# Kernel optimization log

Measured on AMD Instinct MI355X. Metric: run time of the kernel, lower is better.

Reference implementation:

```python
import jax, jax.numpy as jnp
import numpy as np


def setup_inputs() -> dict:
    key = jax.random.key(0)
    bs, width, length = 4, 1536, 2048  # width = 3 * num_heads * ch = 3*8*64
    qkv = jax.random.normal(key, (bs, width, length), dtype=jnp.float32)
    return {"qkv": qkv, "num_heads": 8}


def reference(qkv, num_heads):
    bs, width, length = qkv.shape
    assert width % (3 * num_heads) == 0
    ch = width // (3 * num_heads)
    q, k, v = jnp.split(qkv, 3, axis=1)  # each [bs, num_heads*ch, length]
    scale = 1.0 / np.sqrt(np.sqrt(ch))  # applied to both q and k (total 1/sqrt(ch))
    q = (q * scale).reshape(bs * num_heads, ch, length)
    k = (k * scale).reshape(bs * num_heads, ch, length)
    v = v.reshape(bs * num_heads, ch, length)
    # weight[b, t, s] = sum_c q[b,c,t] * k[b,c,s]
    weight = jnp.einsum('bct,bcs->bts', q, k)
    weight = jax.nn.softmax(weight.astype(jnp.float32), axis=-1).astype(weight.dtype)
    # a[b, c, t] = sum_s weight[b,t,s] * v[b,c,s]
    a = jnp.einsum('bts,bcs->bct', weight, v)
    return a.reshape(bs, num_heads * ch, length)
```

## Files before the change

kernel.cpp:

```cpp
#include <hip/hip_runtime.h>

typedef float f32x16 __attribute__((ext_vector_type(16)));
typedef short short8 __attribute__((ext_vector_type(8)));
typedef unsigned short u16;
typedef unsigned int u32;

#define SEQ_L 2048

#if __has_builtin(__builtin_amdgcn_exp2f)
#define EXP2(x) __builtin_amdgcn_exp2f(x)
#else
#define EXP2(x) exp2f(x)
#endif

__device__ __forceinline__ u32 pk2bf(float lo, float hi) {
#if __has_builtin(__builtin_amdgcn_cvt_pk_bf16_f32)
    typedef __bf16 bf16x2_t __attribute__((ext_vector_type(2)));
    union { bf16x2_t v; u32 i; } w;
    w.v = __builtin_amdgcn_cvt_pk_bf16_f32(lo, hi);
    return w.i;
#else
    union { float f; u32 i; } a, b; a.f = lo; b.f = hi;
    return ((a.i + 0x8000u) >> 16) | ((b.i + 0x8000u) & 0xFFFF0000u);
#endif
}

#define KT_U16 (64 * 64)
#define VT_STRIDE 72
#define VT_U16 (64 * VT_STRIDE)
#define GRP_U16 (KT_U16 + VT_U16)

__global__ __launch_bounds__(512, 4)
void attn_kernel(const float* __restrict__ qkv, float* __restrict__ out) {
    const int tid  = threadIdx.x;
    const int lane = tid & 63;
    const int wv   = tid >> 6;
    const int g    = wv >> 2;
    const int wvin = wv & 3;
    const int col  = lane & 31;
    const int half = lane >> 5;

    const int gid  = blockIdx.x;
    const int head = gid & 31;
    const int tb   = gid >> 5;
    const int t0   = tb * 128 + wvin * 32;
    const int bb   = head >> 3, hh = head & 7;

    const size_t qoff = ((size_t)bb * 1536 + (size_t)hh * 64) * SEQ_L;
    const float* qp = qkv + qoff;
    const float* kp = qp + (size_t)512  * SEQ_L;
    const float* vp = qp + (size_t)1024 * SEQ_L;
    float* op = out + ((size_t)bb * 512 + (size_t)hh * 64) * SEQ_L;

    __shared__ __align__(16) char smem[2 * GRP_U16 * 2];
    u16* ktg = (u16*)smem + g * GRP_U16;
    u16* vtg = ktg + KT_U16;

    const int gtid = tid & 255;
    const int sgrp = gtid & 15;
    const int rq   = gtid >> 4;
    const int sbase0 = g * 1024;

    u16* kw[4];
#pragma unroll
    for (int j = 0; j < 4; ++j) {
        int s = 4 * sgrp + j;
        int sw = ((s >> 2) ^ s) & 7;
        kw[j] = ktg + s * 64 + (((rq >> 1) ^ sw) << 3) + ((rq & 1) << 2);
    }
    const int vcoloff = ((sgrp >> 2) << 4) + ((sgrp & 1) << 3) + (((sgrp >> 1) & 1) << 2);
    u16* vw = vtg + rq * VT_STRIDE + vcoloff;

    const int sw_r = ((col >> 2) ^ col) & 7;
    int kco[4];
#pragma unroll
    for (int ks = 0; ks < 4; ++ks) kco[ks] = ((2 * ks + half) ^ sw_r) << 3;
    const u16* krb0 = ktg + col * 64;
    const u16* krb1 = ktg + (32 + col) * 64;
    const u16* vrb0 = vtg + col * VT_STRIDE + half * 8;
    const u16* vrb1 = vtg + (32 + col) * VT_STRIDE + half * 8;

    const int t = t0 + col;
    const float qscale = 0.18033688f;
    short8 qf[4];
#pragma unroll
    for (int ks = 0; ks < 4; ++ks) {
        union { u32 u[4]; short8 v; } qq;
#pragma unroll
        for (int e2 = 0; e2 < 4; ++e2) {
            int c = ks * 16 + half * 8 + 2 * e2;
            qq.u[e2] = pk2bf(qp[(size_t)c * SEQ_L + t] * qscale,
                             qp[(size_t)(c + 1) * SEQ_L + t] * qscale);
        }
        qf[ks] = qq.v;
    }

    f32x16 zacc;
#pragma unroll
    for (int r = 0; r < 16; ++r) zacc[r] = 0.0f;

    f32x16 accO[2];
#pragma unroll
    for (int m = 0; m < 2; ++m)
#pragma unroll
        for (int r = 0; r < 16; ++r) accO[m][r] = 0.0f;
    float lsum = 0.0f;

    float4 kreg[4], vreg[4];
#pragma unroll
    for (int rr = 0; rr < 4; ++rr) {
        kreg[rr] = *(const float4*)(kp + (size_t)(4 * rq + rr) * SEQ_L + sbase0 + 4 * sgrp);
        vreg[rr] = *(const float4*)(vp + (size_t)(rq + 16 * rr) * SEQ_L + sbase0 + 4 * sgrp);
    }

    for (int it = 0; it < 16; ++it) {
        __syncthreads();
#pragma unroll
        for (int j = 0; j < 4; ++j) {
            uint2 w;
            w.x = pk2bf(kreg[0][j], kreg[1][j]);
            w.y = pk2bf(kreg[2][j], kreg[3][j]);
            *(uint2*)kw[j] = w;
        }
#pragma unroll
        for (int rr = 0; rr < 4; ++rr) {
            uint2 w;
            w.x = pk2bf(vreg[rr].x, vreg[rr].y);
            w.y = pk2bf(vreg[rr].z, vreg[rr].w);
            *(uint2*)(vw + 16 * rr * VT_STRIDE) = w;
        }
        __syncthreads();

        if (it + 1 < 16) {
            const int sn = sbase0 + (it + 1) * 64;
#pragma unroll
            for (int rr = 0; rr < 4; ++rr) {
                kreg[rr] = *(const float4*)(kp + (size_t)(4 * rq + rr) * SEQ_L + sn + 4 * sgrp);
                vreg[rr] = *(const float4*)(vp + (size_t)(rq + 16 * rr) * SEQ_L + sn + 4 * sgrp);
            }
        }

        f32x16 acc[2];
#pragma unroll
        for (int mb = 0; mb < 2; ++mb) {
            const u16* rb = mb ? krb1 : krb0;
            acc[mb] = __builtin_amdgcn_mfma_f32_32x32x16_bf16(
                *(const short8*)(rb + kco[0]), qf[0], zacc, 0, 0, 0);
#pragma unroll
            for (int ks = 1; ks < 4; ++ks)
                acc[mb] = __builtin_amdgcn_mfma_f32_32x32x16_bf16(
                    *(const short8*)(rb + kco[ks]), qf[ks], acc[mb], 0, 0, 0);
        }

        u32 preg[2][8];
#pragma unroll
        for (int mb = 0; mb < 2; ++mb) {
            float p[16];
#pragma unroll
            for (int r = 0; r < 16; ++r) p[r] = EXP2(acc[mb][r]);
            float s0 = ((p[0] + p[1]) + (p[2] + p[3])) + ((p[4] + p[5]) + (p[6] + p[7]));
            float s1 = ((p[8] + p[9]) + (p[10] + p[11])) + ((p[12] + p[13]) + (p[14] + p[15]));
            lsum += s0 + s1;
#pragma unroll
            for (int u2 = 0; u2 < 8; ++u2)
                preg[mb][u2] = pk2bf(p[2 * u2], p[2 * u2 + 1]);
        }

#pragma unroll
        for (int mk = 0; mk < 4; ++mk) {
            int mb = mk >> 1, kb = mk & 1;
            union { u32 u[4]; short8 v; } bfrag;
            bfrag.u[0] = preg[mb][4 * kb + 0];
            bfrag.u[1] = preg[mb][4 * kb + 1];
            bfrag.u[2] = preg[mb][4 * kb + 2];
            bfrag.u[3] = preg[mb][4 * kb + 3];
#pragma unroll
            for (int mbc = 0; mbc < 2; ++mbc) {
                const u16* vb = (mbc ? vrb1 : vrb0) + mk * 16;
                accO[mbc] = __builtin_amdgcn_mfma_f32_32x32x16_bf16(
                    *(const short8*)vb, bfrag.v, accO[mbc], 0, 0, 0);
            }
        }
    }

    __syncthreads();
    float* ep = (float*)smem;
    if (g == 1) {
        float* row = ep + (wvin * 64 + lane) * 33;
#pragma unroll
        for (int mbc = 0; mbc < 2; ++mbc)
#pragma unroll
            for (int r = 0; r < 16; ++r) row[mbc * 16 + r] = accO[mbc][r];
        row[32] = lsum;
    }
    __syncthreads();
    if (g == 0) {
        const float* row = ep + (wvin * 64 + lane) * 33;
#pragma unroll
        for (int mbc = 0; mbc < 2; ++mbc)
#pragma unroll
            for (int r = 0; r < 16; ++r) accO[mbc][r] += row[mbc * 16 + r];
        lsum += row[32];
        float ltot = lsum + __shfl_xor(lsum, 32, 64);
        float inv = 1.0f / ltot;
#pragma unroll
        for (int mbc = 0; mbc < 2; ++mbc) {
#pragma unroll
            for (int r = 0; r < 16; ++r) {
                int c = mbc * 32 + (r & 3) + 8 * (r >> 2) + 4 * half;
                op[(size_t)c * SEQ_L + t] = accO[mbc][r] * inv;
            }
        }
    }
}

extern "C" void kernel_launch(void* const* d_in, const int* in_sizes, int n_in,
                              void* d_out, int out_size, void* d_ws, size_t ws_size,
                              hipStream_t stream) {
    (void)in_sizes; (void)n_in; (void)d_ws; (void)ws_size; (void)out_size;
    const float* qkv = (const float*)d_in[0];
    float* out = (float*)d_out;
    attn_kernel<<<dim3(512), dim3(512), 0, stream>>>(qkv, out);
}
```

Baseline: 128.5 us.

## Double-buffer K/V shared-memory tiles to halve barriers per iteration

Splits the shared-memory K/V staging area into two buffers per group. Each iteration computes from the current buffer and writes the next tile into the other, so the loop needs one barrier per iteration instead of two. Shared memory per block doubles from about 34 KB to about 68 KB, which may lower how many blocks fit on a CU, against the launch bound that asks for 4 blocks.

```diff
diff --git a/kernel.cpp b/kernel.cpp
--- a/kernel.cpp
+++ b/kernel.cpp
@@ -52,33 +52,33 @@
     const float* vp = qp + (size_t)1024 * SEQ_L;
     float* op = out + ((size_t)bb * 512 + (size_t)hh * 64) * SEQ_L;
 
-    __shared__ __align__(16) char smem[2 * GRP_U16 * 2];
-    u16* ktg = (u16*)smem + g * GRP_U16;
-    u16* vtg = ktg + KT_U16;
+    __shared__ __align__(16) u16 smem[2 * 2 * GRP_U16];
+    u16* base0 = smem + g * GRP_U16;
+    u16* base1 = smem + (2 + g) * GRP_U16;
 
     const int gtid = tid & 255;
     const int sgrp = gtid & 15;
     const int rq   = gtid >> 4;
     const int sbase0 = g * 1024;
 
-    u16* kw[4];
+    int kwo[4];
 #pragma unroll
     for (int j = 0; j < 4; ++j) {
         int s = 4 * sgrp + j;
         int sw = ((s >> 2) ^ s) & 7;
-        kw[j] = ktg + s * 64 + (((rq >> 1) ^ sw) << 3) + ((rq & 1) << 2);
+        kwo[j] = s * 64 + (((rq >> 1) ^ sw) << 3) + ((rq & 1) << 2);
     }
     const int vcoloff = ((sgrp >> 2) << 4) + ((sgrp & 1) << 3) + (((sgrp >> 1) & 1) << 2);
-    u16* vw = vtg + rq * VT_STRIDE + vcoloff;
+    const int vwo = KT_U16 + rq * VT_STRIDE + vcoloff;
 
     const int sw_r = ((col >> 2) ^ col) & 7;
     int kco[4];
 #pragma unroll
     for (int ks = 0; ks < 4; ++ks) kco[ks] = ((2 * ks + half) ^ sw_r) << 3;
-    const u16* krb0 = ktg + col * 64;
-    const u16* krb1 = ktg + (32 + col) * 64;
-    const u16* vrb0 = vtg + col * VT_STRIDE + half * 8;
-    const u16* vrb1 = vtg + (32 + col) * VT_STRIDE + half * 8;
+    const int kro0 = col * 64;
+    const int kro1 = (32 + col) * 64;
+    const int vro0 = KT_U16 + col * VT_STRIDE + half * 8;
+    const int vro1 = KT_U16 + (32 + col) * VT_STRIDE + half * 8;
 
     const int t = t0 + col;
     const float qscale = 0.18033688f;
@@ -107,43 +107,44 @@
     float lsum = 0.0f;
 
     float4 kreg[4], vreg[4];
-#pragma unroll
-    for (int rr = 0; rr < 4; ++rr) {
-        kreg[rr] = *(const float4*)(kp + (size_t)(4 * rq + rr) * SEQ_L + sbase0 + 4 * sgrp);
-        vreg[rr] = *(const float4*)(vp + (size_t)(rq + 16 * rr) * SEQ_L + sbase0 + 4 * sgrp);
-    }
-
-    for (int it = 0; it < 16; ++it) {
-        __syncthreads();
+    auto load_tile = [&](int sb) {
+#pragma unroll
+        for (int rr = 0; rr < 4; ++rr) {
+            kreg[rr] = *(const float4*)(kp + (size_t)(4 * rq + rr) * SEQ_L + sb + 4 * sgrp);
+            vreg[rr] = *(const float4*)(vp + (size_t)(rq + 16 * rr) * SEQ_L + sb + 4 * sgrp);
+        }
+    };
+    auto publish = [&](u16* base) {
 #pragma unroll
         for (int j = 0; j < 4; ++j) {
             uint2 w;
             w.x = pk2bf(kreg[0][j], kreg[1][j]);
             w.y = pk2bf(kreg[2][j], kreg[3][j]);
-            *(uint2*)kw[j] = w;
+            *(uint2*)(base + kwo[j]) = w;
         }
 #pragma unroll
         for (int rr = 0; rr < 4; ++rr) {
             uint2 w;
             w.x = pk2bf(vreg[rr].x, vreg[rr].y);
             w.y = pk2bf(vreg[rr].z, vreg[rr].w);
-            *(uint2*)(vw + 16 * rr * VT_STRIDE) = w;
-        }
-        __syncthreads();
-
-        if (it + 1 < 16) {
-            const int sn = sbase0 + (it + 1) * 64;
-#pragma unroll
-            for (int rr = 0; rr < 4; ++rr) {
-                kreg[rr] = *(const float4*)(kp + (size_t)(4 * rq + rr) * SEQ_L + sn + 4 * sgrp);
-                vreg[rr] = *(const float4*)(vp + (size_t)(rq + 16 * rr) * SEQ_L + sn + 4 * sgrp);
-            }
-        }
+            *(uint2*)(base + vwo + 16 * rr * VT_STRIDE) = w;
+        }
+    };
+
+    load_tile(sbase0);
+    publish(base0);
+    __syncthreads();
+
+    for (int it = 0; it < 16; ++it) {
+        u16* cur = (it & 1) ? base1 : base0;
+        u16* nxt = (it & 1) ? base0 : base1;
+
+        if (it + 1 < 16) load_tile(sbase0 + (it + 1) * 64);
 
         f32x16 acc[2];
 #pragma unroll
         for (int mb = 0; mb < 2; ++mb) {
-            const u16* rb = mb ? krb1 : krb0;
+            const u16* rb = cur + (mb ? kro1 : kro0);
             acc[mb] = __builtin_amdgcn_mfma_f32_32x32x16_bf16(
                 *(const short8*)(rb + kco[0]), qf[0], zacc, 0, 0, 0);
 #pragma unroll
@@ -176,14 +177,16 @@
             bfrag.u[3] = preg[mb][4 * kb + 3];
 #pragma unroll
             for (int mbc = 0; mbc < 2; ++mbc) {
-                const u16* vb = (mbc ? vrb1 : vrb0) + mk * 16;
+                const u16* vb = cur + (mbc ? vro1 : vro0) + mk * 16;
                 accO[mbc] = __builtin_amdgcn_mfma_f32_32x32x16_bf16(
                     *(const short8*)vb, bfrag.v, accO[mbc], 0, 0, 0);
             }
         }
-    }
-
-    __syncthreads();
+
+        if (it + 1 < 16) publish(nxt);
+        __syncthreads();
+    }
+
     float* ep = (float*)smem;
     if (g == 1) {
         float* row = ep + (wvin * 64 + lane) * 33;
```

Result: slower. 132.3 us (+3.0%).
